# Optimization experiments

Hardware: AMD Instinct MI355X
Metric: run time of the kernel (lower is better)

The kernel has to match this reference:

```python
import jax, jax.numpy as jnp
import numpy as np

B, F, R, C = 16384, 256, 32, 16
H1, H2 = 128, 32        # FS-MLP hidden sizes
G1, G2 = 256, 64        # consequent MLP hidden sizes


def setup_inputs() -> dict:
    key = jax.random.key(0)
    ks = jax.random.split(key, 16)
    s = 0.05
    return {
        "data": jax.random.normal(ks[0], (B, F), jnp.float32),
        # per-rule antecedent params (torch inits proto=0, var=1; randomize proto for a nontrivial test)
        "proto": jax.random.normal(ks[1], (R, F), jnp.float32) * 0.1,
        "var": jnp.full((R, F), 0.05, jnp.float32),
        # shared FS-MLP: Linear(F,128)->ReLU->Linear(128,32)->ReLU->Linear(32,1)->ReLU
        "Wf1": jax.random.normal(ks[2], (H1, F), jnp.float32) * s,
        "bf1": jax.random.normal(ks[3], (H1,), jnp.float32) * s,
        "Wf2": jax.random.normal(ks[4], (H2, H1), jnp.float32) * s,
        "bf2": jax.random.normal(ks[5], (H2,), jnp.float32) * s,
        "Wf3": jax.random.normal(ks[6], (1, H2), jnp.float32) * s,
        "bf3": jax.random.normal(ks[7], (1,), jnp.float32) * s,
        # per-rule consequent MLP (stacked over rule dim): Linear(F,256)->ELU->Linear(256,64)->ELU->Linear(64,C)
        "Wc1": jax.random.normal(ks[8], (R, G1, F), jnp.float32) * s,
        "bc1": jax.random.normal(ks[9], (R, G1), jnp.float32) * s,
        "Wc2": jax.random.normal(ks[10], (R, G2, G1), jnp.float32) * s,
        "bc2": jax.random.normal(ks[11], (R, G2), jnp.float32) * s,
        "Wc3": jax.random.normal(ks[12], (R, C, G2), jnp.float32) * s,
        "bc3": jax.random.normal(ks[13], (R, C), jnp.float32) * s,
    }


def reference(data, proto, var, Wf1, bf1, Wf2, bf2, Wf3, bf3,
              Wc1, bc1, Wc2, bc2, Wc3, bc3):
    # Antecedent: Gaussian membership per rule -> [R, B, F]
    v = jnp.clip(var, 1e-4, 0.1)
    mem = jnp.exp(-(data[None, :, :] - proto[:, None, :]) ** 2
                  / (2.0 * v[:, None, :] ** 2))
    # Shared firing-strength MLP on each rule's membership tensor -> [R, B]
    h = jax.nn.relu(jnp.einsum('rbf,of->rbo', mem, Wf1) + bf1)
    h = jax.nn.relu(jnp.einsum('rbo,po->rbp', h, Wf2) + bf2)
    fs_ini = jax.nn.relu(jnp.einsum('rbp,qp->rbq', h, Wf3) + bf3)[..., 0]
    fire_strength = jax.nn.softmax(fs_ini.T, axis=1)  # [B, R], softmax over rules
    # Per-rule consequent MLPs on raw data (batched over rule dim) -> [R, B, C]
    c = jax.nn.elu(jnp.einsum('bf,rhf->rbh', data, Wc1) + bc1[:, None, :])
    c = jax.nn.elu(jnp.einsum('rbh,rgh->rbg', c, Wc2) + bc2[:, None, :])
    c = jax.nn.relu(jnp.einsum('rbg,rcg->rbc', c, Wc3) + bc3[:, None, :])
    # Softmax-weighted sum over rules -> [B, C]
    outputs = jnp.einsum('rbc,br->bc', c, fire_strength)
    return outputs, fire_strength
```

## Files before the change

### kernel.cpp

```cpp
#include <hip/hip_runtime.h>
#include <hip/hip_bf16.h>

#define BN 16384
#define FN 256
#define RN 32
#define CN 16
#define H1N 128
#define H2N 32
#define G1N 256
#define G2N 64

typedef __bf16 bf16_t;
typedef __bf16 bf16x8 __attribute__((ext_vector_type(8)));
typedef __bf16 bf16x4 __attribute__((ext_vector_type(4)));
typedef float f32x4 __attribute__((ext_vector_type(4)));

#define OFF_DATA   0UL
#define OFF_WF1    8388608UL
#define OFF_WF2    8454144UL
#define OFF_WC1    8462336UL
#define OFF_WC2    12656640UL
#define OFF_WC3    13705216UL
#define OFF_FSINI  13770752UL
#define OFF_C3     15867904UL

__device__ __forceinline__ f32x4 mfma16(bf16x8 a, bf16x8 b, f32x4 c) {
  return __builtin_amdgcn_mfma_f32_16x16x32_bf16(a, b, c, 0, 0, 0);
}

__device__ __forceinline__ float elu_f(float v) {
  float e = __builtin_amdgcn_exp2f(v * 1.44269504f) - 1.0f;
  return v > 0.f ? v : e;
}

__device__ __forceinline__ bf16x8 lfrag(const char* base, int strideB, int n0, int k0, int lane) {
  int row = n0 + (lane & 15);
  int off = (k0 * 2 + ((lane >> 4) << 4)) ^ ((row & 7) << 4);
  return *(const bf16x8*)(base + row * strideB + off);
}

__device__ __forceinline__ void pack_frag8(const float* __restrict__ src, bf16_t* __restrict__ dst,
                                           int NT, int KS, int g) {
  int per = NT * KS * 64;
  int r = g / per;
  int local = g - r * per;
  int lane = local & 63;
  int fr = local >> 6;
  int ks = fr / NT;
  int nt = fr - ks * NT;
  int N = NT * 16, K = KS * 32;
  int n = nt * 16 + (lane & 15);
  int k = ks * 32 + ((lane >> 4) << 3);
  const float* s = src + (long)r * N * K + (long)n * K + k;
  float4 a = *(const float4*)s;
  float4 b = *(const float4*)(s + 4);
  bf16x8 o;
  o[0] = (bf16_t)a.x; o[1] = (bf16_t)a.y; o[2] = (bf16_t)a.z; o[3] = (bf16_t)a.w;
  o[4] = (bf16_t)b.x; o[5] = (bf16_t)b.y; o[6] = (bf16_t)b.z; o[7] = (bf16_t)b.w;
  *(bf16x8*)(dst + (long)g * 8) = o;
}

#define G_DATA 524288
#define G_WC1  262144
#define G_WC2  65536
#define G_WF1  4096
#define G_WC3  4096
#define G_WF2  512
#define G_TOTAL (G_DATA + G_WC1 + G_WC2 + G_WF1 + G_WC3 + G_WF2)

__global__ __launch_bounds__(256) void k0_pack(
    const float* __restrict__ data, const float* __restrict__ Wf1, const float* __restrict__ Wf2,
    const float* __restrict__ Wc1, const float* __restrict__ Wc2, const float* __restrict__ Wc3,
    char* __restrict__ ws)
{
  int g = blockIdx.x * 256 + threadIdx.x;
  if (g < G_DATA) {
    const float* s = data + (long)g * 8;
    float4 a = *(const float4*)s, b = *(const float4*)(s + 4);
    bf16x8 o;
    o[0] = (bf16_t)a.x; o[1] = (bf16_t)a.y; o[2] = (bf16_t)a.z; o[3] = (bf16_t)a.w;
    o[4] = (bf16_t)b.x; o[5] = (bf16_t)b.y; o[6] = (bf16_t)b.z; o[7] = (bf16_t)b.w;
    *(bf16x8*)((bf16_t*)(ws + OFF_DATA) + (long)g * 8) = o;
    return;
  }
  g -= G_DATA;
  if (g < G_WC1) { pack_frag8(Wc1, (bf16_t*)(ws + OFF_WC1), 16, 8, g); return; }
  g -= G_WC1;
  if (g < G_WC2) { pack_frag8(Wc2, (bf16_t*)(ws + OFF_WC2), 4, 8, g); return; }
  g -= G_WC2;
  if (g < G_WF1) { pack_frag8(Wf1, (bf16_t*)(ws + OFF_WF1), 8, 8, g); return; }
  g -= G_WF1;
  if (g < G_WC3) { pack_frag8(Wc3, (bf16_t*)(ws + OFF_WC3), 1, 2, g); return; }
  g -= G_WC3;
  if (g < G_WF2) { pack_frag8(Wf2, (bf16_t*)(ws + OFF_WF2), 2, 4, g); return; }
}

__device__ __forceinline__ void k1_body(
    char* smem, int bid,
    const float* __restrict__ data, const float* __restrict__ proto, const float* __restrict__ var,
    const float* __restrict__ bf1g, const float* __restrict__ bf2g,
    const float* __restrict__ Wf3g, const float* __restrict__ bf3g,
    const bf16_t* __restrict__ Wf1p, const bf16_t* __restrict__ Wf2p,
    float* __restrict__ fsini)
{
  char* fs_lds   = smem;
  bf16_t* h2t    = (bf16_t*)(smem + 32768);
  float* proto_s = (float*)(smem + 36864);
  float* ivar_s  = (float*)(smem + 37888);

  const int r   = bid >> 8;
  const int b0  = (bid & 255) << 6;
  const int tid = threadIdx.x;
  const int lane = tid & 63;
  const int w   = tid >> 6;

  if (tid < FN) {
    proto_s[tid] = proto[r * FN + tid];
    float v = var[r * FN + tid];
    v = fminf(fmaxf(v, 1e-4f), 0.1f);
    ivar_s[tid] = 1.4426950408889634f * 0.5f / (v * v);
  }
  __syncthreads();

  {
    const int row = tid >> 3;
    const int f0  = (tid & 7) << 5;
    const float* dp = data + (long)(b0 + row) * FN + f0;
    char* mrow = fs_lds + row * 512;
    const int sw = (row & 7) << 4;
    #pragma unroll
    for (int i = 0; i < 4; ++i) {
      const int f = f0 + i * 8;
      float4 x0 = *(const float4*)(dp + i * 8);
      float4 x1 = *(const float4*)(dp + i * 8 + 4);
      bf16x8 m; float d;
      d = x0.x - proto_s[f + 0]; m[0] = (bf16_t)__builtin_amdgcn_exp2f(-d * d * ivar_s[f + 0]);
      d = x0.y - proto_s[f + 1]; m[1] = (bf16_t)__builtin_amdgcn_exp2f(-d * d * ivar_s[f + 1]);
      d = x0.z - proto_s[f + 2]; m[2] = (bf16_t)__builtin_amdgcn_exp2f(-d * d * ivar_s[f + 2]);
      d = x0.w - proto_s[f + 3]; m[3] = (bf16_t)__builtin_amdgcn_exp2f(-d * d * ivar_s[f + 3]);
      d = x1.x - proto_s[f + 4]; m[4] = (bf16_t)__builtin_amdgcn_exp2f(-d * d * ivar_s[f + 4]);
      d = x1.y - proto_s[f + 5]; m[5] = (bf16_t)__builtin_amdgcn_exp2f(-d * d * ivar_s[f + 5]);
      d = x1.z - proto_s[f + 6]; m[6] = (bf16_t)__builtin_amdgcn_exp2f(-d * d * ivar_s[f + 6]);
      d = x1.w - proto_s[f + 7]; m[7] = (bf16_t)__builtin_amdgcn_exp2f(-d * d * ivar_s[f + 7]);
      *(bf16x8*)(mrow + ((f * 2) ^ sw)) = m;
    }
  }
  __syncthreads();

  f32x4 acc[4] = {};
  #pragma unroll
  for (int ks = 0; ks < 8; ++ks) {
    bf16x8 a = *(const bf16x8*)(Wf1p + (((ks * 8 + w) * 64 + lane)) * 8);
    #pragma unroll
    for (int j = 0; j < 4; ++j) {
      bf16x8 bb = lfrag(fs_lds, 512, j * 16, ks * 32, lane);
      acc[j] = mfma16(a, bb, acc[j]);
    }
  }
  __syncthreads();

  {
    const int hb = w * 16 + ((lane >> 4) << 2);
    f32x4 bias = *(const f32x4*)(bf1g + hb);
    #pragma unroll
    for (int j = 0; j < 4; ++j) {
      const int b = j * 16 + (lane & 15);
      bf16x4 o;
      #pragma unroll
      for (int q = 0; q < 4; ++q)
        o[q] = (bf16_t)fmaxf(acc[j][q] + bias[q], 0.f);
      *(bf16x4*)(fs_lds + b * 256 + ((hb * 2) ^ ((b & 7) << 4))) = o;
    }
  }
  __syncthreads();

  {
    const int m = w >> 2;
    const int n = w & 3;
    f32x4 acc2 = {};
    #pragma unroll
    for (int ks = 0; ks < 4; ++ks) {
      bf16x8 a = *(const bf16x8*)(Wf2p + (((ks * 2 + m) * 64 + lane)) * 8);
      bf16x8 bb = lfrag(fs_lds, 256, n * 16, ks * 32, lane);
      acc2 = mfma16(a, bb, acc2);
    }
    const int p0 = m * 16 + ((lane >> 4) << 2);
    const int b  = n * 16 + (lane & 15);
    f32x4 bias = *(const f32x4*)(bf2g + p0);
    #pragma unroll
    for (int q = 0; q < 4; ++q)
      h2t[(p0 + q) * 64 + b] = (bf16_t)fmaxf(acc2[q] + bias[q], 0.f);
  }
  __syncthreads();

  if (tid < 64) {
    float s = bf3g[0];
    #pragma unroll
    for (int p = 0; p < H2N; ++p) s += (float)h2t[p * 64 + tid] * Wf3g[p];
    fsini[(long)(b0 + tid) * RN + r] = fmaxf(s, 0.f);
  }
}

__device__ __forceinline__ void k3_body(
    char* smem, int bid,
    const bf16_t* __restrict__ datab,
    const bf16_t* __restrict__ Wc1p, const bf16_t* __restrict__ Wc2p, const bf16_t* __restrict__ Wc3p,
    const float* __restrict__ bc1, const float* __restrict__ bc2, const float* __restrict__ bc3,
    float* __restrict__ c3buf)
{
  char* a_lds  = smem;
  char* c2_lds = smem + 32768;

  const int xcd = bid & 7;
  const int kk  = bid >> 3;
  const int r   = xcd * 4 + (kk >> 8);
  const int b0  = (kk & 255) << 6;

  const int tid = threadIdx.x;
  const int lane = tid & 63;
  const int w   = tid >> 6;

  {
    const int row = tid >> 3;
    const int e0  = (tid & 7) << 5;
    const bf16_t* sp = datab + (long)(b0 + row) * FN + e0;
    char* drow = a_lds + row * 512;
    const int sw = (row & 7) << 4;
    #pragma unroll
    for (int i = 0; i < 4; ++i) {
      bf16x8 v = *(const bf16x8*)(sp + i * 8);
      *(bf16x8*)(drow + (((e0 + i * 8) * 2) ^ sw)) = v;
    }
  }
  __syncthreads();

  const bf16_t* W1 = Wc1p + (long)r * G1N * FN;
  f32x4 acc[2][4] = {};
  #pragma unroll
  for (int ks = 0; ks < 8; ++ks) {
    bf16x8 a[2], bb[4];
    #pragma unroll
    for (int i = 0; i < 2; ++i)
      a[i] = *(const bf16x8*)(W1 + (((ks * 16 + w * 2 + i) * 64 + lane)) * 8);
    #pragma unroll
    for (int j = 0; j < 4; ++j)
      bb[j] = lfrag(a_lds, 512, j * 16, ks * 32, lane);
    #pragma unroll
    for (int i = 0; i < 2; ++i)
      #pragma unroll
      for (int j = 0; j < 4; ++j)
        acc[i][j] = mfma16(a[i], bb[j], acc[i][j]);
  }
  __syncthreads();

  #pragma unroll
  for (int i = 0; i < 2; ++i) {
    const int g1b = (w * 2 + i) * 16 + ((lane >> 4) << 2);
    f32x4 bias = *(const f32x4*)(bc1 + r * G1N + g1b);
    #pragma unroll
    for (int j = 0; j < 4; ++j) {
      const int b = j * 16 + (lane & 15);
      bf16x4 o;
      #pragma unroll
      for (int q = 0; q < 4; ++q)
        o[q] = (bf16_t)elu_f(acc[i][j][q] + bias[q]);
      *(bf16x4*)(a_lds + b * 512 + ((g1b * 2) ^ ((b & 7) << 4))) = o;
    }
  }
  __syncthreads();

  const int m2 = w >> 1;
  const int n2 = w & 1;
  const bf16_t* W2 = Wc2p + (long)r * G2N * G1N;
  f32x4 acc2[2] = {};
  #pragma unroll
  for (int ks = 0; ks < 8; ++ks) {
    bf16x8 a = *(const bf16x8*)(W2 + (((ks * 4 + m2) * 64 + lane)) * 8);
    #pragma unroll
    for (int j = 0; j < 2; ++j) {
      bf16x8 bb = lfrag(a_lds, 512, (n2 * 2 + j) * 16, ks * 32, lane);
      acc2[j] = mfma16(a, bb, acc2[j]);
    }
  }
  {
    const int g2b = m2 * 16 + ((lane >> 4) << 2);
    f32x4 bias = *(const f32x4*)(bc2 + r * G2N + g2b);
    #pragma unroll
    for (int j = 0; j < 2; ++j) {
      const int b = (n2 * 2 + j) * 16 + (lane & 15);
      bf16x4 o;
      #pragma unroll
      for (int q = 0; q < 4; ++q)
        o[q] = (bf16_t)elu_f(acc2[j][q] + bias[q]);
      *(bf16x4*)(c2_lds + b * 128 + ((g2b * 2) ^ ((b & 7) << 4))) = o;
    }
  }
  __syncthreads();

  if (w < 4) {
    const bf16_t* W3 = Wc3p + (long)r * CN * G2N;
    f32x4 acc3 = {};
    #pragma unroll
    for (int ks = 0; ks < 2; ++ks) {
      bf16x8 a = *(const bf16x8*)(W3 + (((long)ks * 64 + lane)) * 8);
      bf16x8 bb = lfrag(c2_lds, 128, w * 16, ks * 32, lane);
      acc3 = mfma16(a, bb, acc3);
    }
    const int c0 = ((lane >> 4) << 2);
    const int b  = w * 16 + (lane & 15);
    f32x4 bias = *(const f32x4*)(bc3 + r * CN + c0);
    f32x4 o;
    #pragma unroll
    for (int q = 0; q < 4; ++q) o[q] = fmaxf(acc3[q] + bias[q], 0.f);
    *(f32x4*)(c3buf + ((long)r * BN + b0 + b) * CN + c0) = o;
  }
}

__global__ __launch_bounds__(512) void k13_fused(
    const float* __restrict__ data, const float* __restrict__ proto, const float* __restrict__ var,
    const float* __restrict__ bf1g, const float* __restrict__ bf2g,
    const float* __restrict__ Wf3g, const float* __restrict__ bf3g,
    const bf16_t* __restrict__ Wf1p, const bf16_t* __restrict__ Wf2p,
    float* __restrict__ fsini,
    const bf16_t* __restrict__ datab,
    const bf16_t* __restrict__ Wc1p, const bf16_t* __restrict__ Wc2p, const bf16_t* __restrict__ Wc3p,
    const float* __restrict__ bc1, const float* __restrict__ bc2, const float* __restrict__ bc3,
    float* __restrict__ c3buf)
{
  __shared__ __attribute__((aligned(16))) char smem[40960];
  const int bid = blockIdx.x;
  if (bid & 1) {
    k1_body(smem, bid >> 1, data, proto, var, bf1g, bf2g, Wf3g, bf3g, Wf1p, Wf2p, fsini);
  } else {
    k3_body(smem, bid >> 1, datab, Wc1p, Wc2p, Wc3p, bc1, bc2, bc3, c3buf);
  }
}

__global__ __launch_bounds__(256) void k2_softmax(const float* __restrict__ fsini,
                                                  float* __restrict__ fire)
{
  int b = blockIdx.x * 256 + threadIdx.x;
  float v[RN];
  const float4* p = (const float4*)(fsini + (long)b * RN);
  #pragma unroll
  for (int i = 0; i < RN / 4; ++i) {
    float4 t = p[i];
    v[4 * i] = t.x; v[4 * i + 1] = t.y; v[4 * i + 2] = t.z; v[4 * i + 3] = t.w;
  }
  float m = v[0];
  #pragma unroll
  for (int i = 1; i < RN; ++i) m = fmaxf(m, v[i]);
  float s = 0.f;
  #pragma unroll
  for (int i = 0; i < RN; ++i) { v[i] = expf(v[i] - m); s += v[i]; }
  float inv = 1.f / s;
  float4* o = (float4*)(fire + (long)b * RN);
  #pragma unroll
  for (int i = 0; i < RN / 4; ++i) {
    float4 t; t.x = v[4 * i] * inv; t.y = v[4 * i + 1] * inv;
    t.z = v[4 * i + 2] * inv; t.w = v[4 * i + 3] * inv;
    o[i] = t;
  }
}

__global__ __launch_bounds__(256) void k4_out(const float* __restrict__ c3buf,
                                              const float* __restrict__ fire,
                                              float* __restrict__ out)
{
  int t = blockIdx.x * 256 + threadIdx.x;
  int b = t >> 2, c4 = (t & 3) << 2;
  const float* fp = fire + (long)b * RN;
  f32x4 s = {};
  #pragma unroll
  for (int rr = 0; rr < RN; ++rr) {
    float fw = fp[rr];
    f32x4 v = *(const f32x4*)(c3buf + ((long)rr * BN + b) * CN + c4);
    s += fw * v;
  }
  *(f32x4*)(out + (long)b * CN + c4) = s;
}

extern "C" void kernel_launch(void* const* d_in, const int* in_sizes, int n_in,
                              void* d_out, int out_size, void* d_ws, size_t ws_size,
                              hipStream_t stream) {
  const float* data = (const float*)d_in[0];
  const float* proto = (const float*)d_in[1];
  const float* var  = (const float*)d_in[2];
  const float* Wf1  = (const float*)d_in[3];
  const float* bf1  = (const float*)d_in[4];
  const float* Wf2  = (const float*)d_in[5];
  const float* bf2  = (const float*)d_in[6];
  const float* Wf3  = (const float*)d_in[7];
  const float* bf3  = (const float*)d_in[8];
  const float* Wc1  = (const float*)d_in[9];
  const float* bc1  = (const float*)d_in[10];
  const float* Wc2  = (const float*)d_in[11];
  const float* bc2  = (const float*)d_in[12];
  const float* Wc3  = (const float*)d_in[13];
  const float* bc3  = (const float*)d_in[14];

  char* ws = (char*)d_ws;
  bf16_t* datab = (bf16_t*)(ws + OFF_DATA);
  bf16_t* Wf1p  = (bf16_t*)(ws + OFF_WF1);
  bf16_t* Wf2p  = (bf16_t*)(ws + OFF_WF2);
  bf16_t* Wc1p  = (bf16_t*)(ws + OFF_WC1);
  bf16_t* Wc2p  = (bf16_t*)(ws + OFF_WC2);
  bf16_t* Wc3p  = (bf16_t*)(ws + OFF_WC3);
  float*  fsini = (float*)(ws + OFF_FSINI);
  float*  c3buf = (float*)(ws + OFF_C3);

  float* out  = (float*)d_out;
  float* fire = out + (long)BN * CN;

  k0_pack<<<G_TOTAL / 256, 256, 0, stream>>>(data, Wf1, Wf2, Wc1, Wc2, Wc3, ws);
  k13_fused<<<2 * RN * (BN / 64), 512, 0, stream>>>(
      data, proto, var, bf1, bf2, Wf3, bf3, Wf1p, Wf2p, fsini,
      datab, Wc1p, Wc2p, Wc3p, bc1, bc2, bc3, c3buf);
  k2_softmax<<<BN / 256, 256, 0, stream>>>(fsini, fire);
  k4_out<<<(BN * CN / 4) / 256, 256, 0, stream>>>(c3buf, fire, out);
}
```

Before: 251.0 us.

## Halve fused block to 256 threads with larger per-wave MFMA tiles

The fused kernel drops from 512 to 256 threads per block (4 waves), and each wave now computes twice as many output tiles in every GEMM stage: acc[2][4] in the FS layer-1, a 2x2 register tile in the consequent layer-2, and so on. The data/membership staging loops are widened to match. Each B fragment loaded from LDS is now reused across more A fragments, which cuts LDS traffic per MFMA, and launch_bounds(256,4) asks for four resident blocks per CU. The cost is more accumulator registers per thread and fewer waves per block, which can limit occupancy or latency hiding.

```diff
diff --git a/kernel.cpp b/kernel.cpp
--- a/kernel.cpp
+++ b/kernel.cpp
@@ -114,7 +114,7 @@
   const int lane = tid & 63;
   const int w   = tid >> 6;
 
-  if (tid < FN) {
+  {
     proto_s[tid] = proto[r * FN + tid];
     float v = var[r * FN + tid];
     v = fminf(fmaxf(v, 1e-4f), 0.1f);
@@ -123,13 +123,13 @@
   __syncthreads();
 
   {
-    const int row = tid >> 3;
-    const int f0  = (tid & 7) << 5;
+    const int row = tid >> 2;
+    const int f0  = (tid & 3) << 6;
     const float* dp = data + (long)(b0 + row) * FN + f0;
     char* mrow = fs_lds + row * 512;
     const int sw = (row & 7) << 4;
     #pragma unroll
-    for (int i = 0; i < 4; ++i) {
+    for (int i = 0; i < 8; ++i) {
       const int f = f0 + i * 8;
       float4 x0 = *(const float4*)(dp + i * 8);
       float4 x1 = *(const float4*)(dp + i * 8 + 4);
@@ -147,20 +147,27 @@
   }
   __syncthreads();
 
-  f32x4 acc[4] = {};
+  f32x4 acc[2][4] = {};
   #pragma unroll
   for (int ks = 0; ks < 8; ++ks) {
-    bf16x8 a = *(const bf16x8*)(Wf1p + (((ks * 8 + w) * 64 + lane)) * 8);
-    #pragma unroll
-    for (int j = 0; j < 4; ++j) {
-      bf16x8 bb = lfrag(fs_lds, 512, j * 16, ks * 32, lane);
-      acc[j] = mfma16(a, bb, acc[j]);
-    }
-  }
-  __syncthreads();
-
-  {
-    const int hb = w * 16 + ((lane >> 4) << 2);
+    bf16x8 a[2], bb[4];
+    #pragma unroll
+    for (int i = 0; i < 2; ++i)
+      a[i] = *(const bf16x8*)(Wf1p + (((ks * 8 + w * 2 + i) * 64 + lane)) * 8);
+    #pragma unroll
+    for (int j = 0; j < 4; ++j)
+      bb[j] = lfrag(fs_lds, 512, j * 16, ks * 32, lane);
+    #pragma unroll
+    for (int i = 0; i < 2; ++i)
+      #pragma unroll
+      for (int j = 0; j < 4; ++j)
+        acc[i][j] = mfma16(a[i], bb[j], acc[i][j]);
+  }
+  __syncthreads();
+
+  #pragma unroll
+  for (int i = 0; i < 2; ++i) {
+    const int hb = (w * 2 + i) * 16 + ((lane >> 4) << 2);
     f32x4 bias = *(const f32x4*)(bf1g + hb);
     #pragma unroll
     for (int j = 0; j < 4; ++j) {
@@ -168,28 +175,33 @@
       bf16x4 o;
       #pragma unroll
       for (int q = 0; q < 4; ++q)
-        o[q] = (bf16_t)fmaxf(acc[j][q] + bias[q], 0.f);
+        o[q] = (bf16_t)fmaxf(acc[i][j][q] + bias[q], 0.f);
       *(bf16x4*)(fs_lds + b * 256 + ((hb * 2) ^ ((b & 7) << 4))) = o;
     }
   }
   __syncthreads();
 
   {
-    const int m = w >> 2;
-    const int n = w & 3;
-    f32x4 acc2 = {};
+    const int m = w >> 1;
+    f32x4 acc2[2] = {};
     #pragma unroll
     for (int ks = 0; ks < 4; ++ks) {
       bf16x8 a = *(const bf16x8*)(Wf2p + (((ks * 2 + m) * 64 + lane)) * 8);
-      bf16x8 bb = lfrag(fs_lds, 256, n * 16, ks * 32, lane);
-      acc2 = mfma16(a, bb, acc2);
+      #pragma unroll
+      for (int j = 0; j < 2; ++j) {
+        bf16x8 bb = lfrag(fs_lds, 256, ((w & 1) * 2 + j) * 16, ks * 32, lane);
+        acc2[j] = mfma16(a, bb, acc2[j]);
+      }
     }
     const int p0 = m * 16 + ((lane >> 4) << 2);
-    const int b  = n * 16 + (lane & 15);
     f32x4 bias = *(const f32x4*)(bf2g + p0);
     #pragma unroll
-    for (int q = 0; q < 4; ++q)
-      h2t[(p0 + q) * 64 + b] = (bf16_t)fmaxf(acc2[q] + bias[q], 0.f);
+    for (int j = 0; j < 2; ++j) {
+      const int b = ((w & 1) * 2 + j) * 16 + (lane & 15);
+      #pragma unroll
+      for (int q = 0; q < 4; ++q)
+        h2t[(p0 + q) * 64 + b] = (bf16_t)fmaxf(acc2[j][q] + bias[q], 0.f);
+    }
   }
   __syncthreads();
 
@@ -221,13 +233,13 @@
   const int w   = tid >> 6;
 
   {
-    const int row = tid >> 3;
-    const int e0  = (tid & 7) << 5;
+    const int row = tid >> 2;
+    const int e0  = (tid & 3) << 6;
     const bf16_t* sp = datab + (long)(b0 + row) * FN + e0;
     char* drow = a_lds + row * 512;
     const int sw = (row & 7) << 4;
     #pragma unroll
-    for (int i = 0; i < 4; ++i) {
+    for (int i = 0; i < 8; ++i) {
       bf16x8 v = *(const bf16x8*)(sp + i * 8);
       *(bf16x8*)(drow + (((e0 + i * 8) * 2) ^ sw)) = v;
     }
@@ -235,18 +247,18 @@
   __syncthreads();
 
   const bf16_t* W1 = Wc1p + (long)r * G1N * FN;
-  f32x4 acc[2][4] = {};
+  f32x4 acc[4][4] = {};
   #pragma unroll
   for (int ks = 0; ks < 8; ++ks) {
-    bf16x8 a[2], bb[4];
-    #pragma unroll
-    for (int i = 0; i < 2; ++i)
-      a[i] = *(const bf16x8*)(W1 + (((ks * 16 + w * 2 + i) * 64 + lane)) * 8);
+    bf16x8 a[4], bb[4];
+    #pragma unroll
+    for (int i = 0; i < 4; ++i)
+      a[i] = *(const bf16x8*)(W1 + (((ks * 16 + w * 4 + i) * 64 + lane)) * 8);
     #pragma unroll
     for (int j = 0; j < 4; ++j)
       bb[j] = lfrag(a_lds, 512, j * 16, ks * 32, lane);
     #pragma unroll
-    for (int i = 0; i < 2; ++i)
+    for (int i = 0; i < 4; ++i)
       #pragma unroll
       for (int j = 0; j < 4; ++j)
         acc[i][j] = mfma16(a[i], bb[j], acc[i][j]);
@@ -254,8 +266,8 @@
   __syncthreads();
 
   #pragma unroll
-  for (int i = 0; i < 2; ++i) {
-    const int g1b = (w * 2 + i) * 16 + ((lane >> 4) << 2);
+  for (int i = 0; i < 4; ++i) {
+    const int g1b = (w * 4 + i) * 16 + ((lane >> 4) << 2);
     f32x4 bias = *(const f32x4*)(bc1 + r * G1N + g1b);
     #pragma unroll
     for (int j = 0; j < 4; ++j) {
@@ -269,35 +281,40 @@
   }
   __syncthreads();
 
-  const int m2 = w >> 1;
-  const int n2 = w & 1;
   const bf16_t* W2 = Wc2p + (long)r * G2N * G1N;
-  f32x4 acc2[2] = {};
+  f32x4 acc2[2][2] = {};
   #pragma unroll
   for (int ks = 0; ks < 8; ++ks) {
-    bf16x8 a = *(const bf16x8*)(W2 + (((ks * 4 + m2) * 64 + lane)) * 8);
+    bf16x8 a[2], bb[2];
+    #pragma unroll
+    for (int i = 0; i < 2; ++i)
+      a[i] = *(const bf16x8*)(W2 + (((ks * 4 + (w >> 1) * 2 + i) * 64 + lane)) * 8);
+    #pragma unroll
+    for (int j = 0; j < 2; ++j)
+      bb[j] = lfrag(a_lds, 512, ((w & 1) * 2 + j) * 16, ks * 32, lane);
+    #pragma unroll
+    for (int i = 0; i < 2; ++i)
+      #pragma unroll
+      for (int j = 0; j < 2; ++j)
+        acc2[i][j] = mfma16(a[i], bb[j], acc2[i][j]);
+  }
+  #pragma unroll
+  for (int i = 0; i < 2; ++i) {
+    const int g2b = ((w >> 1) * 2 + i) * 16 + ((lane >> 4) << 2);
+    f32x4 bias = *(const f32x4*)(bc2 + r * G2N + g2b);
     #pragma unroll
     for (int j = 0; j < 2; ++j) {
-      bf16x8 bb = lfrag(a_lds, 512, (n2 * 2 + j) * 16, ks * 32, lane);
-      acc2[j] = mfma16(a, bb, acc2[j]);
-    }
-  }
+      const int b = ((w & 1) * 2 + j) * 16 + (lane & 15);
+      bf16x4 o;
+      #pragma unroll
+      for (int q = 0; q < 4; ++q)
+        o[q] = (bf16_t)elu_f(acc2[i][j][q] + bias[q]);
+      *(bf16x4*)(c2_lds + b * 128 + ((g2b * 2) ^ ((b & 7) << 4))) = o;
+    }
+  }
+  __syncthreads();
+
   {
-    const int g2b = m2 * 16 + ((lane >> 4) << 2);
-    f32x4 bias = *(const f32x4*)(bc2 + r * G2N + g2b);
-    #pragma unroll
-    for (int j = 0; j < 2; ++j) {
-      const int b = (n2 * 2 + j) * 16 + (lane & 15);
-      bf16x4 o;
-      #pragma unroll
-      for (int q = 0; q < 4; ++q)
-        o[q] = (bf16_t)elu_f(acc2[j][q] + bias[q]);
-      *(bf16x4*)(c2_lds + b * 128 + ((g2b * 2) ^ ((b & 7) << 4))) = o;
-    }
-  }
-  __syncthreads();
-
-  if (w < 4) {
     const bf16_t* W3 = Wc3p + (long)r * CN * G2N;
     f32x4 acc3 = {};
     #pragma unroll
@@ -316,7 +333,7 @@
   }
 }
 
-__global__ __launch_bounds__(512) void k13_fused(
+__global__ __launch_bounds__(256, 4) void k13_fused(
     const float* __restrict__ data, const float* __restrict__ proto, const float* __restrict__ var,
     const float* __restrict__ bf1g, const float* __restrict__ bf2g,
     const float* __restrict__ Wf3g, const float* __restrict__ bf3g,
@@ -413,7 +430,7 @@
   float* fire = out + (long)BN * CN;
 
   k0_pack<<<G_TOTAL / 256, 256, 0, stream>>>(data, Wf1, Wf2, Wc1, Wc2, Wc3, ws);
-  k13_fused<<<2 * RN * (BN / 64), 512, 0, stream>>>(
+  k13_fused<<<2 * RN * (BN / 64), 256, 0, stream>>>(
       data, proto, var, bf1, bf2, Wf3, bf3, Wf1p, Wf2p, fsini,
       datab, Wc1p, Wc2p, Wc3p, bc1, bc2, bc3, c3buf);
   k2_softmax<<<BN / 256, 256, 0, stream>>>(fsini, fire);
```

Result: slower. 261.1 us (+4.0%).

## Split fused kernel and retile consequent MLP with 32x32 MFMA and 128-row tiles

Applied to the files above, without the earlier changes.

Splits the interleaved k13_fused kernel back into separate firing-strength and consequent kernels. The consequent kernel is rebuilt around 32x32x16 bf16 MFMA with 128-row batch tiles, and its weights are repacked into 32-row fragments. Each weight fragment is now reused across more batch rows and the MFMA issue count drops. In exchange the kernel uses more LDS per block and more accumulator registers, which may lower occupancy, and the two halves no longer run concurrently within one launch.

```diff
diff --git a/kernel.cpp b/kernel.cpp
--- a/kernel.cpp
+++ b/kernel.cpp
@@ -14,6 +14,7 @@
 typedef __bf16 bf16x8 __attribute__((ext_vector_type(8)));
 typedef __bf16 bf16x4 __attribute__((ext_vector_type(4)));
 typedef float f32x4 __attribute__((ext_vector_type(4)));
+typedef float f32x16 __attribute__((ext_vector_type(16)));
 
 #define OFF_DATA   0UL
 #define OFF_WF1    8388608UL
@@ -27,6 +28,9 @@
 __device__ __forceinline__ f32x4 mfma16(bf16x8 a, bf16x8 b, f32x4 c) {
   return __builtin_amdgcn_mfma_f32_16x16x32_bf16(a, b, c, 0, 0, 0);
 }
+__device__ __forceinline__ f32x16 mfma32(bf16x8 a, bf16x8 b, f32x16 c) {
+  return __builtin_amdgcn_mfma_f32_32x32x16_bf16(a, b, c, 0, 0, 0);
+}
 
 __device__ __forceinline__ float elu_f(float v) {
   float e = __builtin_amdgcn_exp2f(v * 1.44269504f) - 1.0f;
@@ -36,6 +40,12 @@
 __device__ __forceinline__ bf16x8 lfrag(const char* base, int strideB, int n0, int k0, int lane) {
   int row = n0 + (lane & 15);
   int off = (k0 * 2 + ((lane >> 4) << 4)) ^ ((row & 7) << 4);
+  return *(const bf16x8*)(base + row * strideB + off);
+}
+
+__device__ __forceinline__ bf16x8 lfrag32(const char* base, int strideB, int n0, int k0, int lane) {
+  int row = n0 + (lane & 31);
+  int off = (k0 * 2 + ((lane >> 5) << 4)) ^ ((row & 15) << 4);
   return *(const bf16x8*)(base + row * strideB + off);
 }
 
@@ -60,6 +70,27 @@
   *(bf16x8*)(dst + (long)g * 8) = o;
 }
 
+__device__ __forceinline__ void pack_frag32(const float* __restrict__ src, bf16_t* __restrict__ dst,
+                                            int MT, int KS, int g) {
+  int per = MT * KS * 64;
+  int r = g / per;
+  int local = g - r * per;
+  int lane = local & 63;
+  int fr = local >> 6;
+  int ks = fr / MT;
+  int mt = fr - ks * MT;
+  int N = MT * 32, K = KS * 16;
+  int n = mt * 32 + (lane & 31);
+  int k = ks * 16 + ((lane >> 5) << 3);
+  const float* s = src + (long)r * N * K + (long)n * K + k;
+  float4 a = *(const float4*)s;
+  float4 b = *(const float4*)(s + 4);
+  bf16x8 o;
+  o[0] = (bf16_t)a.x; o[1] = (bf16_t)a.y; o[2] = (bf16_t)a.z; o[3] = (bf16_t)a.w;
+  o[4] = (bf16_t)b.x; o[5] = (bf16_t)b.y; o[6] = (bf16_t)b.z; o[7] = (bf16_t)b.w;
+  *(bf16x8*)(dst + (long)g * 8) = o;
+}
+
 #define G_DATA 524288
 #define G_WC1  262144
 #define G_WC2  65536
@@ -84,9 +115,9 @@
     return;
   }
   g -= G_DATA;
-  if (g < G_WC1) { pack_frag8(Wc1, (bf16_t*)(ws + OFF_WC1), 16, 8, g); return; }
+  if (g < G_WC1) { pack_frag32(Wc1, (bf16_t*)(ws + OFF_WC1), 8, 16, g); return; }
   g -= G_WC1;
-  if (g < G_WC2) { pack_frag8(Wc2, (bf16_t*)(ws + OFF_WC2), 4, 8, g); return; }
+  if (g < G_WC2) { pack_frag32(Wc2, (bf16_t*)(ws + OFF_WC2), 2, 16, g); return; }
   g -= G_WC2;
   if (g < G_WF1) { pack_frag8(Wf1, (bf16_t*)(ws + OFF_WF1), 8, 8, g); return; }
   g -= G_WF1;
@@ -95,19 +126,20 @@
   if (g < G_WF2) { pack_frag8(Wf2, (bf16_t*)(ws + OFF_WF2), 2, 4, g); return; }
 }
 
-__device__ __forceinline__ void k1_body(
-    char* smem, int bid,
+__global__ __launch_bounds__(512) void k1_fs(
     const float* __restrict__ data, const float* __restrict__ proto, const float* __restrict__ var,
     const float* __restrict__ bf1g, const float* __restrict__ bf2g,
     const float* __restrict__ Wf3g, const float* __restrict__ bf3g,
     const bf16_t* __restrict__ Wf1p, const bf16_t* __restrict__ Wf2p,
     float* __restrict__ fsini)
 {
+  __shared__ __attribute__((aligned(16))) char smem[38912];
   char* fs_lds   = smem;
   bf16_t* h2t    = (bf16_t*)(smem + 32768);
   float* proto_s = (float*)(smem + 36864);
   float* ivar_s  = (float*)(smem + 37888);
 
+  const int bid = blockIdx.x;
   const int r   = bid >> 8;
   const int b0  = (bid & 255) << 6;
   const int tid = threadIdx.x;
@@ -201,141 +233,6 @@
   }
 }
 
-__device__ __forceinline__ void k3_body(
-    char* smem, int bid,
-    const bf16_t* __restrict__ datab,
-    const bf16_t* __restrict__ Wc1p, const bf16_t* __restrict__ Wc2p, const bf16_t* __restrict__ Wc3p,
-    const float* __restrict__ bc1, const float* __restrict__ bc2, const float* __restrict__ bc3,
-    float* __restrict__ c3buf)
-{
-  char* a_lds  = smem;
-  char* c2_lds = smem + 32768;
-
-  const int xcd = bid & 7;
-  const int kk  = bid >> 3;
-  const int r   = xcd * 4 + (kk >> 8);
-  const int b0  = (kk & 255) << 6;
-
-  const int tid = threadIdx.x;
-  const int lane = tid & 63;
-  const int w   = tid >> 6;
-
-  {
-    const int row = tid >> 3;
-    const int e0  = (tid & 7) << 5;
-    const bf16_t* sp = datab + (long)(b0 + row) * FN + e0;
-    char* drow = a_lds + row * 512;
-    const int sw = (row & 7) << 4;
-    #pragma unroll
-    for (int i = 0; i < 4; ++i) {
-      bf16x8 v = *(const bf16x8*)(sp + i * 8);
-      *(bf16x8*)(drow + (((e0 + i * 8) * 2) ^ sw)) = v;
-    }
-  }
-  __syncthreads();
-
-  const bf16_t* W1 = Wc1p + (long)r * G1N * FN;
-  f32x4 acc[2][4] = {};
-  #pragma unroll
-  for (int ks = 0; ks < 8; ++ks) {
-    bf16x8 a[2], bb[4];
-    #pragma unroll
-    for (int i = 0; i < 2; ++i)
-      a[i] = *(const bf16x8*)(W1 + (((ks * 16 + w * 2 + i) * 64 + lane)) * 8);
-    #pragma unroll
-    for (int j = 0; j < 4; ++j)
-      bb[j] = lfrag(a_lds, 512, j * 16, ks * 32, lane);
-    #pragma unroll
-    for (int i = 0; i < 2; ++i)
-      #pragma unroll
-      for (int j = 0; j < 4; ++j)
-        acc[i][j] = mfma16(a[i], bb[j], acc[i][j]);
-  }
-  __syncthreads();
-
-  #pragma unroll
-  for (int i = 0; i < 2; ++i) {
-    const int g1b = (w * 2 + i) * 16 + ((lane >> 4) << 2);
-    f32x4 bias = *(const f32x4*)(bc1 + r * G1N + g1b);
-    #pragma unroll
-    for (int j = 0; j < 4; ++j) {
-      const int b = j * 16 + (lane & 15);
-      bf16x4 o;
-      #pragma unroll
-      for (int q = 0; q < 4; ++q)
-        o[q] = (bf16_t)elu_f(acc[i][j][q] + bias[q]);
-      *(bf16x4*)(a_lds + b * 512 + ((g1b * 2) ^ ((b & 7) << 4))) = o;
-    }
-  }
-  __syncthreads();
-
-  const int m2 = w >> 1;
-  const int n2 = w & 1;
-  const bf16_t* W2 = Wc2p + (long)r * G2N * G1N;
-  f32x4 acc2[2] = {};
-  #pragma unroll
-  for (int ks = 0; ks < 8; ++ks) {
-    bf16x8 a = *(const bf16x8*)(W2 + (((ks * 4 + m2) * 64 + lane)) * 8);
-    #pragma unroll
-    for (int j = 0; j < 2; ++j) {
-      bf16x8 bb = lfrag(a_lds, 512, (n2 * 2 + j) * 16, ks * 32, lane);
-      acc2[j] = mfma16(a, bb, acc2[j]);
-    }
-  }
-  {
-    const int g2b = m2 * 16 + ((lane >> 4) << 2);
-    f32x4 bias = *(const f32x4*)(bc2 + r * G2N + g2b);
-    #pragma unroll
-    for (int j = 0; j < 2; ++j) {
-      const int b = (n2 * 2 + j) * 16 + (lane & 15);
-      bf16x4 o;
-      #pragma unroll
-      for (int q = 0; q < 4; ++q)
-        o[q] = (bf16_t)elu_f(acc2[j][q] + bias[q]);
-      *(bf16x4*)(c2_lds + b * 128 + ((g2b * 2) ^ ((b & 7) << 4))) = o;
-    }
-  }
-  __syncthreads();
-
-  if (w < 4) {
-    const bf16_t* W3 = Wc3p + (long)r * CN * G2N;
-    f32x4 acc3 = {};
-    #pragma unroll
-    for (int ks = 0; ks < 2; ++ks) {
-      bf16x8 a = *(const bf16x8*)(W3 + (((long)ks * 64 + lane)) * 8);
-      bf16x8 bb = lfrag(c2_lds, 128, w * 16, ks * 32, lane);
-      acc3 = mfma16(a, bb, acc3);
-    }
-    const int c0 = ((lane >> 4) << 2);
-    const int b  = w * 16 + (lane & 15);
-    f32x4 bias = *(const f32x4*)(bc3 + r * CN + c0);
-    f32x4 o;
-    #pragma unroll
-    for (int q = 0; q < 4; ++q) o[q] = fmaxf(acc3[q] + bias[q], 0.f);
-    *(f32x4*)(c3buf + ((long)r * BN + b0 + b) * CN + c0) = o;
-  }
-}
-
-__global__ __launch_bounds__(512) void k13_fused(
-    const float* __restrict__ data, const float* __restrict__ proto, const float* __restrict__ var,
-    const float* __restrict__ bf1g, const float* __restrict__ bf2g,
-    const float* __restrict__ Wf3g, const float* __restrict__ bf3g,
-    const bf16_t* __restrict__ Wf1p, const bf16_t* __restrict__ Wf2p,
-    float* __restrict__ fsini,
-    const bf16_t* __restrict__ datab,
-    const bf16_t* __restrict__ Wc1p, const bf16_t* __restrict__ Wc2p, const bf16_t* __restrict__ Wc3p,
-    const float* __restrict__ bc1, const float* __restrict__ bc2, const float* __restrict__ bc3,
-    float* __restrict__ c3buf)
-{
-  __shared__ __attribute__((aligned(16))) char smem[40960];
-  const int bid = blockIdx.x;
-  if (bid & 1) {
-    k1_body(smem, bid >> 1, data, proto, var, bf1g, bf2g, Wf3g, bf3g, Wf1p, Wf2p, fsini);
-  } else {
-    k3_body(smem, bid >> 1, datab, Wc1p, Wc2p, Wc3p, bc1, bc2, bc3, c3buf);
-  }
-}
-
 __global__ __launch_bounds__(256) void k2_softmax(const float* __restrict__ fsini,
                                                   float* __restrict__ fire)
 {
@@ -360,6 +257,129 @@
     float4 t; t.x = v[4 * i] * inv; t.y = v[4 * i + 1] * inv;
     t.z = v[4 * i + 2] * inv; t.w = v[4 * i + 3] * inv;
     o[i] = t;
+  }
+}
+
+__global__ __launch_bounds__(512, 4) void k3_cons(
+    const bf16_t* __restrict__ datab,
+    const bf16_t* __restrict__ Wc1p, const bf16_t* __restrict__ Wc2p, const bf16_t* __restrict__ Wc3p,
+    const float* __restrict__ bc1, const float* __restrict__ bc2, const float* __restrict__ bc3,
+    float* __restrict__ c3buf)
+{
+  __shared__ __attribute__((aligned(16))) char a_lds[65536];
+  __shared__ __attribute__((aligned(16))) char c2_lds[16384];
+
+  const int bid = blockIdx.x;
+  const int xcd = bid & 7;
+  const int kk  = bid >> 3;
+  const int r   = xcd * 4 + (kk >> 7);
+  const int b0  = (kk & 127) << 7;
+
+  const int tid = threadIdx.x;
+  const int lane = tid & 63;
+  const int w   = tid >> 6;
+
+  {
+    const int row = tid >> 2;
+    const int e0  = (tid & 3) << 6;
+    const bf16_t* sp = datab + (long)(b0 + row) * FN + e0;
+    char* drow = a_lds + row * 512;
+    const int sw = (row & 15) << 4;
+    #pragma unroll
+    for (int i = 0; i < 8; ++i) {
+      bf16x8 v = *(const bf16x8*)(sp + i * 8);
+      *(bf16x8*)(drow + (((e0 + i * 8) * 2) ^ sw)) = v;
+    }
+  }
+  __syncthreads();
+
+  const int wm = w >> 1;
+  const int wn = w & 1;
+  const bf16_t* W1 = Wc1p + (long)r * G1N * FN;
+  f32x16 acc[2][2] = {};
+  #pragma unroll
+  for (int ks = 0; ks < 16; ++ks) {
+    bf16x8 a[2], bb[2];
+    #pragma unroll
+    for (int i = 0; i < 2; ++i)
+      a[i] = *(const bf16x8*)(W1 + (((ks * 8 + wm * 2 + i) * 64 + lane)) * 8);
+    #pragma unroll
+    for (int j = 0; j < 2; ++j)
+      bb[j] = lfrag32(a_lds, 512, (wn * 2 + j) * 32, ks * 16, lane);
+    #pragma unroll
+    for (int i = 0; i < 2; ++i)
+      #pragma unroll
+      for (int j = 0; j < 2; ++j)
+        acc[i][j] = mfma32(a[i], bb[j], acc[i][j]);
+  }
+  __syncthreads();
+
+  #pragma unroll
+  for (int i = 0; i < 2; ++i) {
+    const int m0 = (wm * 2 + i) * 32;
+    #pragma unroll
+    for (int j = 0; j < 2; ++j) {
+      const int b = (wn * 2 + j) * 32 + (lane & 31);
+      char* brow = a_lds + b * 512;
+      const int sw = (b & 15) << 4;
+      #pragma unroll
+      for (int grp = 0; grp < 4; ++grp) {
+        const int g1 = m0 + grp * 8 + ((lane >> 5) << 2);
+        f32x4 bias = *(const f32x4*)(bc1 + r * G1N + g1);
+        bf16x4 o;
+        #pragma unroll
+        for (int q = 0; q < 4; ++q)
+          o[q] = (bf16_t)elu_f(acc[i][j][grp * 4 + q] + bias[q]);
+        *(bf16x4*)(brow + ((g1 * 2) ^ sw)) = o;
+      }
+    }
+  }
+  __syncthreads();
+
+  const int m2 = w >> 2;
+  const int n2 = w & 3;
+  const bf16_t* W2 = Wc2p + (long)r * G2N * G1N;
+  f32x16 acc2 = {};
+  #pragma unroll
+  for (int ks = 0; ks < 16; ++ks) {
+    bf16x8 a = *(const bf16x8*)(W2 + (((ks * 2 + m2) * 64 + lane)) * 8);
+    bf16x8 bb = lfrag32(a_lds, 512, n2 * 32, ks * 16, lane);
+    acc2 = mfma32(a, bb, acc2);
+  }
+  {
+    const int m0 = m2 * 32;
+    const int b = n2 * 32 + (lane & 31);
+    char* brow = c2_lds + b * 128;
+    const int sw = (b & 7) << 4;
+    #pragma unroll
+    for (int grp = 0; grp < 4; ++grp) {
+      const int g2 = m0 + grp * 8 + ((lane >> 5) << 2);
+      f32x4 bias = *(const f32x4*)(bc2 + r * G2N + g2);
+      bf16x4 o;
+      #pragma unroll
+      for (int q = 0; q < 4; ++q)
+        o[q] = (bf16_t)elu_f(acc2[grp * 4 + q] + bias[q]);
+      *(bf16x4*)(brow + ((g2 * 2) ^ sw)) = o;
+    }
+  }
+  __syncthreads();
+
+  {
+    const bf16_t* W3 = Wc3p + (long)r * CN * G2N;
+    f32x4 acc3 = {};
+    #pragma unroll
+    for (int ks = 0; ks < 2; ++ks) {
+      bf16x8 a = *(const bf16x8*)(W3 + (((long)ks * 64 + lane)) * 8);
+      bf16x8 bb = lfrag(c2_lds, 128, w * 16, ks * 32, lane);
+      acc3 = mfma16(a, bb, acc3);
+    }
+    const int c0 = ((lane >> 4) << 2);
+    const int b  = w * 16 + (lane & 15);
+    f32x4 bias = *(const f32x4*)(bc3 + r * CN + c0);
+    f32x4 o;
+    #pragma unroll
+    for (int q = 0; q < 4; ++q) o[q] = fmaxf(acc3[q] + bias[q], 0.f);
+    *(f32x4*)(c3buf + ((long)r * BN + b0 + b) * CN + c0) = o;
   }
 }
 
@@ -413,9 +433,9 @@
   float* fire = out + (long)BN * CN;
 
   k0_pack<<<G_TOTAL / 256, 256, 0, stream>>>(data, Wf1, Wf2, Wc1, Wc2, Wc3, ws);
-  k13_fused<<<2 * RN * (BN / 64), 512, 0, stream>>>(
-      data, proto, var, bf1, bf2, Wf3, bf3, Wf1p, Wf2p, fsini,
-      datab, Wc1p, Wc2p, Wc3p, bc1, bc2, bc3, c3buf);
+  k3_cons<<<RN * (BN / 128), 512, 0, stream>>>(datab, Wc1p, Wc2p, Wc3p, bc1, bc2, bc3, c3buf);
+  k1_fs<<<RN * (BN / 64), 512, 0, stream>>>(data, proto, var, bf1, bf2, Wf3, bf3,
+                                            Wf1p, Wf2p, fsini);
   k2_softmax<<<BN / 256, 256, 0, stream>>>(fsini, fire);
   k4_out<<<(BN * CN / 4) / 256, 256, 0, stream>>>(c3buf, fire, out);
 }
```

New measurement: 297.1 us. +18.4%, slower.

## Split fused k1/k3 kernel, process two rules per consequent block, fuse softmax into output

Applied to the files above, without the earlier changes.

Splits the interleaved firing-strength/consequent kernel back into two separate kernels. The consequent kernel now loads the data tile once into LDS and reuses it for two rules, with separate LDS buffers for the layer-1 and layer-2 activations. The softmax is folded into the output-reduction kernel, which removes one launch and the round trip of the fire tensor through memory. In exchange, each consequent block uses more LDS (72KB), which lowers occupancy, and the two branches no longer overlap within a single launch.

```diff
diff --git a/kernel.cpp b/kernel.cpp
--- a/kernel.cpp
+++ b/kernel.cpp
@@ -95,19 +95,20 @@
   if (g < G_WF2) { pack_frag8(Wf2, (bf16_t*)(ws + OFF_WF2), 2, 4, g); return; }
 }
 
-__device__ __forceinline__ void k1_body(
-    char* smem, int bid,
+__global__ __launch_bounds__(512) void k1_fs(
     const float* __restrict__ data, const float* __restrict__ proto, const float* __restrict__ var,
     const float* __restrict__ bf1g, const float* __restrict__ bf2g,
     const float* __restrict__ Wf3g, const float* __restrict__ bf3g,
     const bf16_t* __restrict__ Wf1p, const bf16_t* __restrict__ Wf2p,
     float* __restrict__ fsini)
 {
+  __shared__ __attribute__((aligned(16))) char smem[38912];
   char* fs_lds   = smem;
   bf16_t* h2t    = (bf16_t*)(smem + 32768);
   float* proto_s = (float*)(smem + 36864);
   float* ivar_s  = (float*)(smem + 37888);
 
+  const int bid = blockIdx.x;
   const int r   = bid >> 8;
   const int b0  = (bid & 255) << 6;
   const int tid = threadIdx.x;
@@ -201,19 +202,21 @@
   }
 }
 
-__device__ __forceinline__ void k3_body(
-    char* smem, int bid,
+__global__ __launch_bounds__(512) void k3_cons(
     const bf16_t* __restrict__ datab,
     const bf16_t* __restrict__ Wc1p, const bf16_t* __restrict__ Wc2p, const bf16_t* __restrict__ Wc3p,
     const float* __restrict__ bc1, const float* __restrict__ bc2, const float* __restrict__ bc3,
     float* __restrict__ c3buf)
 {
-  char* a_lds  = smem;
-  char* c2_lds = smem + 32768;
-
+  __shared__ __attribute__((aligned(16))) char smem[73728];
+  char* d_lds  = smem;
+  char* c1_lds = smem + 32768;
+  char* c2_lds = smem + 65536;
+
+  const int bid = blockIdx.x;
   const int xcd = bid & 7;
   const int kk  = bid >> 3;
-  const int r   = xcd * 4 + (kk >> 8);
+  const int rp  = xcd * 2 + (kk >> 8);
   const int b0  = (kk & 255) << 6;
 
   const int tid = threadIdx.x;
@@ -224,7 +227,7 @@
     const int row = tid >> 3;
     const int e0  = (tid & 7) << 5;
     const bf16_t* sp = datab + (long)(b0 + row) * FN + e0;
-    char* drow = a_lds + row * 512;
+    char* drow = d_lds + row * 512;
     const int sw = (row & 7) << 4;
     #pragma unroll
     for (int i = 0; i < 4; ++i) {
@@ -234,150 +237,131 @@
   }
   __syncthreads();
 
-  const bf16_t* W1 = Wc1p + (long)r * G1N * FN;
-  f32x4 acc[2][4] = {};
-  #pragma unroll
-  for (int ks = 0; ks < 8; ++ks) {
-    bf16x8 a[2], bb[4];
-    #pragma unroll
-    for (int i = 0; i < 2; ++i)
-      a[i] = *(const bf16x8*)(W1 + (((ks * 16 + w * 2 + i) * 64 + lane)) * 8);
-    #pragma unroll
-    for (int j = 0; j < 4; ++j)
-      bb[j] = lfrag(a_lds, 512, j * 16, ks * 32, lane);
-    #pragma unroll
-    for (int i = 0; i < 2; ++i)
+  for (int rr = 0; rr < 2; ++rr) {
+    const int r = rp * 2 + rr;
+
+    const bf16_t* W1 = Wc1p + (long)r * G1N * FN;
+    f32x4 acc[2][4] = {};
+    #pragma unroll
+    for (int ks = 0; ks < 8; ++ks) {
+      bf16x8 a[2], bb[4];
+      #pragma unroll
+      for (int i = 0; i < 2; ++i)
+        a[i] = *(const bf16x8*)(W1 + (((ks * 16 + w * 2 + i) * 64 + lane)) * 8);
       #pragma unroll
       for (int j = 0; j < 4; ++j)
-        acc[i][j] = mfma16(a[i], bb[j], acc[i][j]);
-  }
-  __syncthreads();
-
-  #pragma unroll
-  for (int i = 0; i < 2; ++i) {
-    const int g1b = (w * 2 + i) * 16 + ((lane >> 4) << 2);
-    f32x4 bias = *(const f32x4*)(bc1 + r * G1N + g1b);
-    #pragma unroll
-    for (int j = 0; j < 4; ++j) {
-      const int b = j * 16 + (lane & 15);
-      bf16x4 o;
-      #pragma unroll
-      for (int q = 0; q < 4; ++q)
-        o[q] = (bf16_t)elu_f(acc[i][j][q] + bias[q]);
-      *(bf16x4*)(a_lds + b * 512 + ((g1b * 2) ^ ((b & 7) << 4))) = o;
-    }
-  }
-  __syncthreads();
-
-  const int m2 = w >> 1;
-  const int n2 = w & 1;
-  const bf16_t* W2 = Wc2p + (long)r * G2N * G1N;
-  f32x4 acc2[2] = {};
-  #pragma unroll
-  for (int ks = 0; ks < 8; ++ks) {
-    bf16x8 a = *(const bf16x8*)(W2 + (((ks * 4 + m2) * 64 + lane)) * 8);
-    #pragma unroll
-    for (int j = 0; j < 2; ++j) {
-      bf16x8 bb = lfrag(a_lds, 512, (n2 * 2 + j) * 16, ks * 32, lane);
-      acc2[j] = mfma16(a, bb, acc2[j]);
-    }
-  }
-  {
-    const int g2b = m2 * 16 + ((lane >> 4) << 2);
-    f32x4 bias = *(const f32x4*)(bc2 + r * G2N + g2b);
-    #pragma unroll
-    for (int j = 0; j < 2; ++j) {
-      const int b = (n2 * 2 + j) * 16 + (lane & 15);
-      bf16x4 o;
-      #pragma unroll
-      for (int q = 0; q < 4; ++q)
-        o[q] = (bf16_t)elu_f(acc2[j][q] + bias[q]);
-      *(bf16x4*)(c2_lds + b * 128 + ((g2b * 2) ^ ((b & 7) << 4))) = o;
-    }
-  }
-  __syncthreads();
-
-  if (w < 4) {
-    const bf16_t* W3 = Wc3p + (long)r * CN * G2N;
-    f32x4 acc3 = {};
-    #pragma unroll
-    for (int ks = 0; ks < 2; ++ks) {
-      bf16x8 a = *(const bf16x8*)(W3 + (((long)ks * 64 + lane)) * 8);
-      bf16x8 bb = lfrag(c2_lds, 128, w * 16, ks * 32, lane);
-      acc3 = mfma16(a, bb, acc3);
-    }
-    const int c0 = ((lane >> 4) << 2);
-    const int b  = w * 16 + (lane & 15);
-    f32x4 bias = *(const f32x4*)(bc3 + r * CN + c0);
-    f32x4 o;
-    #pragma unroll
-    for (int q = 0; q < 4; ++q) o[q] = fmaxf(acc3[q] + bias[q], 0.f);
-    *(f32x4*)(c3buf + ((long)r * BN + b0 + b) * CN + c0) = o;
-  }
-}
-
-__global__ __launch_bounds__(512) void k13_fused(
-    const float* __restrict__ data, const float* __restrict__ proto, const float* __restrict__ var,
-    const float* __restrict__ bf1g, const float* __restrict__ bf2g,
-    const float* __restrict__ Wf3g, const float* __restrict__ bf3g,
-    const bf16_t* __restrict__ Wf1p, const bf16_t* __restrict__ Wf2p,
-    float* __restrict__ fsini,
-    const bf16_t* __restrict__ datab,
-    const bf16_t* __restrict__ Wc1p, const bf16_t* __restrict__ Wc2p, const bf16_t* __restrict__ Wc3p,
-    const float* __restrict__ bc1, const float* __restrict__ bc2, const float* __restrict__ bc3,
-    float* __restrict__ c3buf)
-{
-  __shared__ __attribute__((aligned(16))) char smem[40960];
-  const int bid = blockIdx.x;
-  if (bid & 1) {
-    k1_body(smem, bid >> 1, data, proto, var, bf1g, bf2g, Wf3g, bf3g, Wf1p, Wf2p, fsini);
-  } else {
-    k3_body(smem, bid >> 1, datab, Wc1p, Wc2p, Wc3p, bc1, bc2, bc3, c3buf);
-  }
-}
-
-__global__ __launch_bounds__(256) void k2_softmax(const float* __restrict__ fsini,
-                                                  float* __restrict__ fire)
-{
-  int b = blockIdx.x * 256 + threadIdx.x;
-  float v[RN];
-  const float4* p = (const float4*)(fsini + (long)b * RN);
-  #pragma unroll
-  for (int i = 0; i < RN / 4; ++i) {
-    float4 t = p[i];
-    v[4 * i] = t.x; v[4 * i + 1] = t.y; v[4 * i + 2] = t.z; v[4 * i + 3] = t.w;
-  }
-  float m = v[0];
-  #pragma unroll
-  for (int i = 1; i < RN; ++i) m = fmaxf(m, v[i]);
-  float s = 0.f;
-  #pragma unroll
-  for (int i = 0; i < RN; ++i) { v[i] = expf(v[i] - m); s += v[i]; }
-  float inv = 1.f / s;
-  float4* o = (float4*)(fire + (long)b * RN);
-  #pragma unroll
-  for (int i = 0; i < RN / 4; ++i) {
-    float4 t; t.x = v[4 * i] * inv; t.y = v[4 * i + 1] * inv;
-    t.z = v[4 * i + 2] * inv; t.w = v[4 * i + 3] * inv;
-    o[i] = t;
-  }
-}
-
-__global__ __launch_bounds__(256) void k4_out(const float* __restrict__ c3buf,
-                                              const float* __restrict__ fire,
-                                              float* __restrict__ out)
+        bb[j] = lfrag(d_lds, 512, j * 16, ks * 32, lane);
+      #pragma unroll
+      for (int i = 0; i < 2; ++i)
+        #pragma unroll
+        for (int j = 0; j < 4; ++j)
+          acc[i][j] = mfma16(a[i], bb[j], acc[i][j]);
+    }
+    #pragma unroll
+    for (int i = 0; i < 2; ++i) {
+      const int g1b = (w * 2 + i) * 16 + ((lane >> 4) << 2);
+      f32x4 bias = *(const f32x4*)(bc1 + r * G1N + g1b);
+      #pragma unroll
+      for (int j = 0; j < 4; ++j) {
+        const int b = j * 16 + (lane & 15);
+        bf16x4 o;
+        #pragma unroll
+        for (int q = 0; q < 4; ++q)
+          o[q] = (bf16_t)elu_f(acc[i][j][q] + bias[q]);
+        *(bf16x4*)(c1_lds + b * 512 + ((g1b * 2) ^ ((b & 7) << 4))) = o;
+      }
+    }
+    __syncthreads();
+
+    {
+      const int m2 = w >> 1;
+      const int n2 = w & 1;
+      const bf16_t* W2 = Wc2p + (long)r * G2N * G1N;
+      f32x4 acc2[2] = {};
+      #pragma unroll
+      for (int ks = 0; ks < 8; ++ks) {
+        bf16x8 a = *(const bf16x8*)(W2 + (((ks * 4 + m2) * 64 + lane)) * 8);
+        #pragma unroll
+        for (int j = 0; j < 2; ++j) {
+          bf16x8 bb = lfrag(c1_lds, 512, (n2 * 2 + j) * 16, ks * 32, lane);
+          acc2[j] = mfma16(a, bb, acc2[j]);
+        }
+      }
+      const int g2b = m2 * 16 + ((lane >> 4) << 2);
+      f32x4 bias = *(const f32x4*)(bc2 + r * G2N + g2b);
+      #pragma unroll
+      for (int j = 0; j < 2; ++j) {
+        const int b = (n2 * 2 + j) * 16 + (lane & 15);
+        bf16x4 o;
+        #pragma unroll
+        for (int q = 0; q < 4; ++q)
+          o[q] = (bf16_t)elu_f(acc2[j][q] + bias[q]);
+        *(bf16x4*)(c2_lds + b * 128 + ((g2b * 2) ^ ((b & 7) << 4))) = o;
+      }
+    }
+    __syncthreads();
+
+    if (w < 4) {
+      const bf16_t* W3 = Wc3p + (long)r * CN * G2N;
+      f32x4 acc3 = {};
+      #pragma unroll
+      for (int ks = 0; ks < 2; ++ks) {
+        bf16x8 a = *(const bf16x8*)(W3 + (((long)ks * 64 + lane)) * 8);
+        bf16x8 bb = lfrag(c2_lds, 128, w * 16, ks * 32, lane);
+        acc3 = mfma16(a, bb, acc3);
+      }
+      const int c0 = ((lane >> 4) << 2);
+      const int b  = w * 16 + (lane & 15);
+      f32x4 bias = *(const f32x4*)(bc3 + r * CN + c0);
+      f32x4 o;
+      #pragma unroll
+      for (int q = 0; q < 4; ++q) o[q] = fmaxf(acc3[q] + bias[q], 0.f);
+      *(f32x4*)(c3buf + ((long)r * BN + b0 + b) * CN + c0) = o;
+    }
+    __syncthreads();
+  }
+}
+
+__global__ __launch_bounds__(256) void k4_out(const float* __restrict__ fsini,
+                                              const float* __restrict__ c3buf,
+                                              float* __restrict__ out,
+                                              float* __restrict__ fire_g)
 {
   int t = blockIdx.x * 256 + threadIdx.x;
   int b = t >> 2, c4 = (t & 3) << 2;
-  const float* fp = fire + (long)b * RN;
-  f32x4 s = {};
-  #pragma unroll
-  for (int rr = 0; rr < RN; ++rr) {
-    float fw = fp[rr];
-    f32x4 v = *(const f32x4*)(c3buf + ((long)rr * BN + b) * CN + c4);
-    s += fw * v;
-  }
-  *(f32x4*)(out + (long)b * CN + c4) = s;
+  float v[RN];
+  const float4* p = (const float4*)(fsini + (long)b * RN);
+  #pragma unroll
+  for (int i = 0; i < RN / 4; ++i) {
+    float4 x = p[i];
+    v[4 * i] = x.x; v[4 * i + 1] = x.y; v[4 * i + 2] = x.z; v[4 * i + 3] = x.w;
+  }
+  float m = v[0];
+  #pragma unroll
+  for (int i = 1; i < RN; ++i) m = fmaxf(m, v[i]);
+  float s = 0.f;
+  #pragma unroll
+  for (int i = 0; i < RN; ++i) { v[i] = expf(v[i] - m); s += v[i]; }
+  float inv = 1.f / s;
+  #pragma unroll
+  for (int i = 0; i < RN; ++i) v[i] *= inv;
+
+  f32x4 acc = {};
+  #pragma unroll
+  for (int rrr = 0; rrr < RN; ++rrr) {
+    f32x4 c = *(const f32x4*)(c3buf + ((long)rrr * BN + b) * CN + c4);
+    acc += v[rrr] * c;
+  }
+  *(f32x4*)(out + (long)b * CN + c4) = acc;
+
+  if (c4 == 0) {
+    float4* o = (float4*)(fire_g + (long)b * RN);
+    #pragma unroll
+    for (int i = 0; i < RN / 4; ++i) {
+      float4 x; x.x = v[4 * i]; x.y = v[4 * i + 1]; x.z = v[4 * i + 2]; x.w = v[4 * i + 3];
+      o[i] = x;
+    }
+  }
 }
 
 extern "C" void kernel_launch(void* const* d_in, const int* in_sizes, int n_in,
@@ -413,9 +397,9 @@
   float* fire = out + (long)BN * CN;
 
   k0_pack<<<G_TOTAL / 256, 256, 0, stream>>>(data, Wf1, Wf2, Wc1, Wc2, Wc3, ws);
-  k13_fused<<<2 * RN * (BN / 64), 512, 0, stream>>>(
-      data, proto, var, bf1, bf2, Wf3, bf3, Wf1p, Wf2p, fsini,
-      datab, Wc1p, Wc2p, Wc3p, bc1, bc2, bc3, c3buf);
-  k2_softmax<<<BN / 256, 256, 0, stream>>>(fsini, fire);
-  k4_out<<<(BN * CN / 4) / 256, 256, 0, stream>>>(c3buf, fire, out);
-}
+  k3_cons<<<16 * (BN / 64) / 2 * 2, 512, 0, stream>>>(datab, Wc1p, Wc2p, Wc3p,
+                                                      bc1, bc2, bc3, c3buf);
+  k1_fs<<<RN * (BN / 64), 512, 0, stream>>>(data, proto, var, bf1, bf2, Wf3, bf3,
+                                            Wf1p, Wf2p, fsini);
+  k4_out<<<(BN * CN / 4) / 256, 256, 0, stream>>>(fsini, c3buf, out, fire);
+}
```

After: 256.2 us. +2.0%, slower.
